# Kernel optimization log

Hardware: AMD Instinct MI355X
Metric: run time of the kernel (lower is better)

## Reference

```python
import jax, jax.numpy as jnp
import numpy as np

# Dimensions (match init_kwargs / input_specs)
B, T, HW, K, J = 8192, 64, 8, 64, 3
FILT_LEN = 8
NEG_SLOPE = 0.001
DWT_OUT_LEN = 84  # lo(14) + hi1(35) + hi2(21) + hi3(14)

# db4 analysis filters (pywt dec_lo / dec_hi)
DB4_LO = np.array([-0.010597401784997278, 0.032883011666982945,
                   0.030841381835986965, -0.18703481171888114,
                   -0.02798376941698385, 0.6308807679295904,
                   0.7148465705525415, 0.23037781330885523], dtype=np.float32)
DB4_HI = np.array([-0.23037781330885523, 0.7148465705525415,
                   -0.6308807679295904, -0.02798376941698385,
                   0.18703481171888114, 0.030841381835986965,
                   0.032883011666982945, -0.010597401784997278], dtype=np.float32)
# pytorch_wavelets stores filters reversed and uses conv1d (cross-correlation)
_H = jnp.asarray(np.ascontiguousarray(np.stack([DB4_LO[::-1], DB4_HI[::-1]])[:, None, :]))  # [2,1,8]


def _afb1d(x):
    # Single-level analysis filter bank along last axis, reflect padding, stride 2.
    # x: [N, n] -> (lo, hi) each [N, floor((n+7)/2)]
    n = x.shape[-1]
    out = (n + FILT_LEN - 1) // 2
    p = 2 * (out - 1) - n + FILT_LEN
    xp = jnp.pad(x, ((0, 0), (p // 2, (p + 1) // 2)), mode='reflect')
    y = jax.lax.conv_general_dilated(xp[:, None, :], _H, (2,), 'VALID')  # [N,2,out]
    return y[:, 0], y[:, 1]


def _dwt(x):
    # J-level DWT; concat [lo_J, hi_1, hi_2, ..., hi_J] along last axis -> [N, 84]
    lo, his = x, []
    for _ in range(J):
        lo, hi = _afb1d(lo)
        his.append(hi)
    return jnp.concatenate([lo] + his, axis=-1)


def setup_inputs() -> dict:
    key = jax.random.key(0)
    k1, k2 = jax.random.split(key)
    x = jax.random.normal(k1, (B, 1, T, HW, HW), dtype=jnp.float32)
    fan_in = DWT_OUT_LEN * HW * HW
    conv_w = jax.random.normal(k2, (K, DWT_OUT_LEN, HW, HW), dtype=jnp.float32) / np.sqrt(fan_in).astype(np.float32)
    conv_b = jnp.zeros((K,), dtype=jnp.float32)
    return {"x": x, "conv_w": conv_w, "conv_b": conv_b}


def reference(x, conv_w, conv_b):
    # x: [B,1,T,H,W]; time_interval=1 and spatial_maxpool_size=1 -> no-ops.
    b = x.shape[0]
    # DWT along time for every (batch, spatial) signal, fully batched.
    sig = x[:, 0].transpose(0, 2, 3, 1).reshape(b * HW * HW, T)  # [B*H*W, T]
    coeffs = _dwt(sig).reshape(b, HW, HW, DWT_OUT_LEN)           # [B,H,W,84]
    # Conv3d with kernel covering the full (84,8,8) volume == one GEMM per output channel.
    feat = jnp.einsum('bhwt,kthw->bk', coeffs, conv_w) + conv_b  # [B,K]
    # Dropout3d in eval mode is identity; LeakyReLU then flatten -> [B, K]
    return jnp.where(feat >= 0, feat, NEG_SLOPE * feat)
```

## Files before the change

kernel.cpp:

```cpp
#include <hip/hip_runtime.h>
#include <hip/hip_bf16.h>

typedef __attribute__((ext_vector_type(4))) float floatx4;
typedef __attribute__((ext_vector_type(8))) short shortx8;

__device__ __constant__ float DLO[8] = {
    -0.010597401784997278f, 0.032883011666982945f,
     0.030841381835986965f, -0.18703481171888114f,
    -0.02798376941698385f,  0.6308807679295904f,
     0.7148465705525415f,   0.23037781330885523f};
__device__ __constant__ float DHI[8] = {
    -0.23037781330885523f,  0.7148465705525415f,
    -0.6308807679295904f,  -0.02798376941698385f,
     0.18703481171888114f,  0.030841381835986965f,
     0.032883011666982945f, -0.010597401784997278f};

__device__ __forceinline__ unsigned short f2bf_rne(float f) {
  unsigned u = __builtin_bit_cast(unsigned, f);
  unsigned r = (u + 0x7FFFu + ((u >> 16) & 1u)) >> 16;
  return (unsigned short)r;
}

template <int N, int OUT>
__device__ __forceinline__ void afb(const float* x, float* lo, float* hi) {
#pragma unroll
  for (int m = 0; m < OUT; ++m) {
    float aL = 0.f, aH = 0.f;
#pragma unroll
    for (int i = 0; i < 8; ++i) {
      int s = 2 * m + 1 - i;
      s = (s < 0) ? -s : s;
      s = (s >= N) ? (2 * N - 2 - s) : s;
      float v = x[s];
      aL = fmaf(DLO[i], v, aL);
      aH = fmaf(DHI[i], v, aH);
    }
    lo[m] = aL; hi[m] = aH;
  }
}

__global__ void build_M_kernel(float* __restrict__ M) {
  const int i = threadIdx.x;
  float sig[64];
#pragma unroll
  for (int t = 0; t < 64; ++t) sig[t] = (t == i) ? 1.f : 0.f;
  float lo1[35], hi1[35], lo2[21], hi2[21], lo3[14], hi3[14];
  afb<64, 35>(sig, lo1, hi1);
  afb<35, 21>(lo1, lo2, hi2);
  afb<21, 14>(lo2, lo3, hi3);
#pragma unroll
  for (int t = 0; t < 14; ++t) M[t * 64 + i] = lo3[t];
#pragma unroll
  for (int t = 0; t < 35; ++t) M[(14 + t) * 64 + i] = hi1[t];
#pragma unroll
  for (int t = 0; t < 21; ++t) M[(49 + t) * 64 + i] = hi2[t];
#pragma unroll
  for (int t = 0; t < 14; ++t) M[(70 + t) * 64 + i] = hi3[t];
}

__global__ __launch_bounds__(256) void build_w2_kernel(
    const float* __restrict__ M, const float* __restrict__ cw,
    unsigned short* __restrict__ W2) {
  __shared__ float Ml[84 * 64];
  __shared__ float Cl[84 * 64];
  const int k = blockIdx.x;
  const float* cwk = cw + (size_t)k * (84 * 64);
  for (int idx = threadIdx.x; idx < 84 * 64; idx += 256) {
    Ml[idx] = M[idx];
    Cl[idx] = cwk[idx];
  }
  __syncthreads();
  const int tp  = blockIdx.y * 16 + (threadIdx.x >> 4);
  const int hw0 = (threadIdx.x & 15) * 4;
  float a0 = 0.f, a1 = 0.f, a2 = 0.f, a3 = 0.f;
#pragma unroll 4
  for (int t = 0; t < 84; ++t) {
    const float mv = Ml[t * 64 + tp];
    const float4 cv = *(const float4*)&Cl[t * 64 + hw0];
    a0 = fmaf(mv, cv.x, a0);
    a1 = fmaf(mv, cv.y, a1);
    a2 = fmaf(mv, cv.z, a2);
    a3 = fmaf(mv, cv.w, a3);
  }
  uint2 pk;
  pk.x = (unsigned)f2bf_rne(a0) | ((unsigned)f2bf_rne(a1) << 16);
  pk.y = (unsigned)f2bf_rne(a2) | ((unsigned)f2bf_rne(a3) << 16);
  *(uint2*)(W2 + (size_t)k * 4096 + tp * 64 + hw0) = pk;
}

#define BM 32
#define BN 64
#define BK 128
#define LDK 136
#define NITER 32

__global__ __launch_bounds__(512) void gemm_kernel(
    const float* __restrict__ A, const unsigned short* __restrict__ W2,
    const float* __restrict__ bias, float* __restrict__ out) {
  __shared__ alignas(16) short As[2][BM * LDK];
  __shared__ alignas(16) short Bs[2][BN * LDK];

  const int tid = threadIdx.x;
  const int b0 = blockIdx.x * BM;

  const int ar = tid >> 4;
  const int ac = (tid & 15) * 8;
  const int bn = tid >> 3;
  const int bc = (tid & 7) * 16;

  const float* aptr = A + (size_t)(b0 + ar) * 4096 + ac;
  const unsigned short* bptr = W2 + (size_t)bn * 4096 + bc;

  const int lane = tid & 63;
  const int wave = tid >> 6;
  const int mt = wave >> 2;
  const int nt = wave & 3;
  const int frow = lane & 15;
  const int fk = (lane >> 4) * 8;

  floatx4 acc = {0.f, 0.f, 0.f, 0.f};

  float4 a0_0 = *(const float4*)(aptr + 0);
  float4 a1_0 = *(const float4*)(aptr + 4);
  uint4  b0_0 = *(const uint4*)(bptr + 0);
  uint4  b1_0 = *(const uint4*)(bptr + 8);
  float4 a0_1 = *(const float4*)(aptr + BK);
  float4 a1_1 = *(const float4*)(aptr + BK + 4);
  uint4  b0_1 = *(const uint4*)(bptr + BK);
  uint4  b1_1 = *(const uint4*)(bptr + BK + 8);

#define GSTEP(S, I)                                                          \
  do {                                                                       \
    shortx8 av;                                                              \
    av[0] = (short)f2bf_rne(a0_##S.x); av[1] = (short)f2bf_rne(a0_##S.y);    \
    av[2] = (short)f2bf_rne(a0_##S.z); av[3] = (short)f2bf_rne(a0_##S.w);    \
    av[4] = (short)f2bf_rne(a1_##S.x); av[5] = (short)f2bf_rne(a1_##S.y);    \
    av[6] = (short)f2bf_rne(a1_##S.z); av[7] = (short)f2bf_rne(a1_##S.w);    \
    *(shortx8*)&As[S][ar * LDK + ac] = av;                                   \
    *(uint4*)&Bs[S][bn * LDK + bc] = b0_##S;                                 \
    *(uint4*)&Bs[S][bn * LDK + bc + 8] = b1_##S;                             \
    __asm__ __volatile__("s_waitcnt lgkmcnt(0)\n\ts_barrier" ::: "memory");  \
    if ((I) + 2 < NITER) {                                                   \
      const int c2 = ((I) + 2) * BK;                                         \
      a0_##S = *(const float4*)(aptr + c2);                                  \
      a1_##S = *(const float4*)(aptr + c2 + 4);                              \
      b0_##S = *(const uint4*)(bptr + c2);                                   \
      b1_##S = *(const uint4*)(bptr + c2 + 8);                               \
    }                                                                        \
    _Pragma("unroll")                                                        \
    for (int kk = 0; kk < 4; ++kk) {                                         \
      shortx8 af = *(const shortx8*)&As[S][(mt * 16 + frow) * LDK + kk * 32 + fk]; \
      shortx8 bf = *(const shortx8*)&Bs[S][(nt * 16 + frow) * LDK + kk * 32 + fk]; \
      acc = __builtin_amdgcn_mfma_f32_16x16x32_bf16(af, bf, acc, 0, 0, 0);   \
    }                                                                        \
  } while (0)

  for (int i = 0; i < NITER; i += 2) {
    GSTEP(0, i);
    GSTEP(1, i + 1);
  }
#undef GSTEP

  const int ocol = nt * 16 + (lane & 15);
  const int orow0 = b0 + mt * 16 + (lane >> 4) * 4;
  const float bv = bias[ocol];
#pragma unroll
  for (int r = 0; r < 4; ++r) {
    float v = acc[r] + bv;
    out[(size_t)(orow0 + r) * 64 + ocol] = (v >= 0.f) ? v : 1.0e-3f * v;
  }
}

extern "C" void kernel_launch(void* const* d_in, const int* in_sizes, int n_in,
                              void* d_out, int out_size, void* d_ws, size_t ws_size,
                              hipStream_t stream) {
  const float* x      = (const float*)d_in[0];
  const float* conv_w = (const float*)d_in[1];
  const float* conv_b = (const float*)d_in[2];
  float* out = (float*)d_out;

  float* Mws = (float*)d_ws;
  unsigned short* W2 = (unsigned short*)((char*)d_ws + 32768);

  build_M_kernel<<<1, 64, 0, stream>>>(Mws);
  build_w2_kernel<<<dim3(64, 4), 256, 0, stream>>>(Mws, conv_w, W2);
  gemm_kernel<<<256, 512, 0, stream>>>(x, W2, conv_b, out);
}
```

Before: 202.8 us.

## Precompute DWT matrix at compile time and use split-K register-direct MFMA GEMM

The DWT basis matrix is now built as a constexpr table in constant memory, so the build_M kernel launch and its global round trip go away. The GEMM is restructured so each 256-thread block handles 16 rows, and its four waves each take a quarter of K. Operands are loaded straight from global memory into MFMA registers, with no LDS staging and no per-step barriers. Partial sums are reduced once through LDS at the end. The change trades LDS tiling for more redundant global reads of W2 (from cache) and a lower in-flight prefetch depth.

New measurement: 220.3 us. +8.7%, slower.

```diff
diff --git a/kernel.cpp b/kernel.cpp
--- a/kernel.cpp
+++ b/kernel.cpp
@@ -4,16 +4,53 @@
 typedef __attribute__((ext_vector_type(4))) float floatx4;
 typedef __attribute__((ext_vector_type(8))) short shortx8;
 
-__device__ __constant__ float DLO[8] = {
+constexpr float CLO[8] = {
     -0.010597401784997278f, 0.032883011666982945f,
      0.030841381835986965f, -0.18703481171888114f,
     -0.02798376941698385f,  0.6308807679295904f,
      0.7148465705525415f,   0.23037781330885523f};
-__device__ __constant__ float DHI[8] = {
+constexpr float CHI[8] = {
     -0.23037781330885523f,  0.7148465705525415f,
     -0.6308807679295904f,  -0.02798376941698385f,
      0.18703481171888114f,  0.030841381835986965f,
      0.032883011666982945f, -0.010597401784997278f};
+
+template <int N, int OUT>
+constexpr void afb_c(const float* x, float* lo, float* hi) {
+  for (int m = 0; m < OUT; ++m) {
+    float aL = 0.f, aH = 0.f;
+    for (int i = 0; i < 8; ++i) {
+      int s = 2 * m + 1 - i;
+      s = (s < 0) ? -s : s;
+      s = (s >= N) ? (2 * N - 2 - s) : s;
+      aL += CLO[i] * x[s];
+      aH += CHI[i] * x[s];
+    }
+    lo[m] = aL; hi[m] = aH;
+  }
+}
+
+struct MTab { float v[84][64]; };
+
+constexpr MTab make_M() {
+  MTab t{};
+  for (int c = 0; c < 64; ++c) {
+    float sig[64] = {};
+    sig[c] = 1.f;
+    float lo1[35] = {}, hi1[35] = {}, lo2[21] = {}, hi2[21] = {};
+    float lo3[14] = {}, hi3[14] = {};
+    afb_c<64, 35>(sig, lo1, hi1);
+    afb_c<35, 21>(lo1, lo2, hi2);
+    afb_c<21, 14>(lo2, lo3, hi3);
+    for (int m = 0; m < 14; ++m) t.v[m][c]      = lo3[m];
+    for (int m = 0; m < 35; ++m) t.v[14 + m][c] = hi1[m];
+    for (int m = 0; m < 21; ++m) t.v[49 + m][c] = hi2[m];
+    for (int m = 0; m < 14; ++m) t.v[70 + m][c] = hi3[m];
+  }
+  return t;
+}
+
+__device__ __constant__ MTab M_TAB = make_M();
 
 __device__ __forceinline__ unsigned short f2bf_rne(float f) {
   unsigned u = __builtin_bit_cast(unsigned, f);
@@ -21,61 +58,19 @@
   return (unsigned short)r;
 }
 
-template <int N, int OUT>
-__device__ __forceinline__ void afb(const float* x, float* lo, float* hi) {
-#pragma unroll
-  for (int m = 0; m < OUT; ++m) {
-    float aL = 0.f, aH = 0.f;
-#pragma unroll
-    for (int i = 0; i < 8; ++i) {
-      int s = 2 * m + 1 - i;
-      s = (s < 0) ? -s : s;
-      s = (s >= N) ? (2 * N - 2 - s) : s;
-      float v = x[s];
-      aL = fmaf(DLO[i], v, aL);
-      aH = fmaf(DHI[i], v, aH);
-    }
-    lo[m] = aL; hi[m] = aH;
-  }
-}
-
-__global__ void build_M_kernel(float* __restrict__ M) {
-  const int i = threadIdx.x;
-  float sig[64];
-#pragma unroll
-  for (int t = 0; t < 64; ++t) sig[t] = (t == i) ? 1.f : 0.f;
-  float lo1[35], hi1[35], lo2[21], hi2[21], lo3[14], hi3[14];
-  afb<64, 35>(sig, lo1, hi1);
-  afb<35, 21>(lo1, lo2, hi2);
-  afb<21, 14>(lo2, lo3, hi3);
-#pragma unroll
-  for (int t = 0; t < 14; ++t) M[t * 64 + i] = lo3[t];
-#pragma unroll
-  for (int t = 0; t < 35; ++t) M[(14 + t) * 64 + i] = hi1[t];
-#pragma unroll
-  for (int t = 0; t < 21; ++t) M[(49 + t) * 64 + i] = hi2[t];
-#pragma unroll
-  for (int t = 0; t < 14; ++t) M[(70 + t) * 64 + i] = hi3[t];
-}
-
 __global__ __launch_bounds__(256) void build_w2_kernel(
-    const float* __restrict__ M, const float* __restrict__ cw,
-    unsigned short* __restrict__ W2) {
-  __shared__ float Ml[84 * 64];
+    const float* __restrict__ cw, unsigned short* __restrict__ W2) {
   __shared__ float Cl[84 * 64];
   const int k = blockIdx.x;
   const float* cwk = cw + (size_t)k * (84 * 64);
-  for (int idx = threadIdx.x; idx < 84 * 64; idx += 256) {
-    Ml[idx] = M[idx];
-    Cl[idx] = cwk[idx];
-  }
+  for (int idx = threadIdx.x; idx < 84 * 64; idx += 256) Cl[idx] = cwk[idx];
   __syncthreads();
   const int tp  = blockIdx.y * 16 + (threadIdx.x >> 4);
   const int hw0 = (threadIdx.x & 15) * 4;
   float a0 = 0.f, a1 = 0.f, a2 = 0.f, a3 = 0.f;
 #pragma unroll 4
   for (int t = 0; t < 84; ++t) {
-    const float mv = Ml[t * 64 + tp];
+    const float mv = M_TAB.v[t][tp];
     const float4 cv = *(const float4*)&Cl[t * 64 + hw0];
     a0 = fmaf(mv, cv.x, a0);
     a1 = fmaf(mv, cv.y, a1);
@@ -88,87 +83,78 @@
   *(uint2*)(W2 + (size_t)k * 4096 + tp * 64 + hw0) = pk;
 }
 
-#define BM 32
-#define BN 64
-#define BK 128
-#define LDK 136
-#define NITER 32
+#define KQ_LEN 1024
+#define KCHUNK 32
 
-__global__ __launch_bounds__(512) void gemm_kernel(
+__global__ __launch_bounds__(256, 2) void gemm_kernel(
     const float* __restrict__ A, const unsigned short* __restrict__ W2,
     const float* __restrict__ bias, float* __restrict__ out) {
-  __shared__ alignas(16) short As[2][BM * LDK];
-  __shared__ alignas(16) short Bs[2][BN * LDK];
+  __shared__ float part[4 * 64 * 16];
 
-  const int tid = threadIdx.x;
-  const int b0 = blockIdx.x * BM;
+  const int tid  = threadIdx.x;
+  const int lane = tid & 63;
+  const int kq   = tid >> 6;
+  const int frow = lane & 15;
+  const int kg   = lane >> 4;
 
-  const int ar = tid >> 4;
-  const int ac = (tid & 15) * 8;
-  const int bn = tid >> 3;
-  const int bc = (tid & 7) * 16;
+  const float* aptr =
+      A + (size_t)(blockIdx.x * 16 + frow) * 4096 + kq * KQ_LEN + kg * 8;
+  const unsigned short* bptr =
+      W2 + (size_t)frow * 4096 + kq * KQ_LEN + kg * 8;
 
-  const float* aptr = A + (size_t)(b0 + ar) * 4096 + ac;
-  const unsigned short* bptr = W2 + (size_t)bn * 4096 + bc;
+  floatx4 acc0 = {0.f, 0.f, 0.f, 0.f};
+  floatx4 acc1 = {0.f, 0.f, 0.f, 0.f};
+  floatx4 acc2 = {0.f, 0.f, 0.f, 0.f};
+  floatx4 acc3 = {0.f, 0.f, 0.f, 0.f};
 
-  const int lane = tid & 63;
-  const int wave = tid >> 6;
-  const int mt = wave >> 2;
-  const int nt = wave & 3;
-  const int frow = lane & 15;
-  const int fk = (lane >> 4) * 8;
+#pragma unroll 2
+  for (int i = 0; i < KQ_LEN / KCHUNK; ++i) {
+    const int off = i * KCHUNK;
+    float4 a0 = *(const float4*)(aptr + off);
+    float4 a1 = *(const float4*)(aptr + off + 4);
+    uint4 bv0 = *(const uint4*)(bptr + off);
+    uint4 bv1 = *(const uint4*)(bptr + 16 * 4096 + off);
+    uint4 bv2 = *(const uint4*)(bptr + 32 * 4096 + off);
+    uint4 bv3 = *(const uint4*)(bptr + 48 * 4096 + off);
+    shortx8 af;
+    af[0] = (short)f2bf_rne(a0.x); af[1] = (short)f2bf_rne(a0.y);
+    af[2] = (short)f2bf_rne(a0.z); af[3] = (short)f2bf_rne(a0.w);
+    af[4] = (short)f2bf_rne(a1.x); af[5] = (short)f2bf_rne(a1.y);
+    af[6] = (short)f2bf_rne(a1.z); af[7] = (short)f2bf_rne(a1.w);
+    acc0 = __builtin_amdgcn_mfma_f32_16x16x32_bf16(
+        af, __builtin_bit_cast(shortx8, bv0), acc0, 0, 0, 0);
+    acc1 = __builtin_amdgcn_mfma_f32_16x16x32_bf16(
+        af, __builtin_bit_cast(shortx8, bv1), acc1, 0, 0, 0);
+    acc2 = __builtin_amdgcn_mfma_f32_16x16x32_bf16(
+        af, __builtin_bit_cast(shortx8, bv2), acc2, 0, 0, 0);
+    acc3 = __builtin_amdgcn_mfma_f32_16x16x32_bf16(
+        af, __builtin_bit_cast(shortx8, bv3), acc3, 0, 0, 0);
+  }
 
-  floatx4 acc = {0.f, 0.f, 0.f, 0.f};
+  float* pp = &part[(kq * 64 + lane) * 16];
+  *(floatx4*)(pp + 0)  = acc0;
+  *(floatx4*)(pp + 4)  = acc1;
+  *(floatx4*)(pp + 8)  = acc2;
+  *(floatx4*)(pp + 12) = acc3;
+  __syncthreads();
 
-  float4 a0_0 = *(const float4*)(aptr + 0);
-  float4 a1_0 = *(const float4*)(aptr + 4);
-  uint4  b0_0 = *(const uint4*)(bptr + 0);
-  uint4  b1_0 = *(const uint4*)(bptr + 8);
-  float4 a0_1 = *(const float4*)(aptr + BK);
-  float4 a1_1 = *(const float4*)(aptr + BK + 4);
-  uint4  b0_1 = *(const uint4*)(bptr + BK);
-  uint4  b1_1 = *(const uint4*)(bptr + BK + 8);
-
-#define GSTEP(S, I)                                                          \
-  do {                                                                       \
-    shortx8 av;                                                              \
-    av[0] = (short)f2bf_rne(a0_##S.x); av[1] = (short)f2bf_rne(a0_##S.y);    \
-    av[2] = (short)f2bf_rne(a0_##S.z); av[3] = (short)f2bf_rne(a0_##S.w);    \
-    av[4] = (short)f2bf_rne(a1_##S.x); av[5] = (short)f2bf_rne(a1_##S.y);    \
-    av[6] = (short)f2bf_rne(a1_##S.z); av[7] = (short)f2bf_rne(a1_##S.w);    \
-    *(shortx8*)&As[S][ar * LDK + ac] = av;                                   \
-    *(uint4*)&Bs[S][bn * LDK + bc] = b0_##S;                                 \
-    *(uint4*)&Bs[S][bn * LDK + bc + 8] = b1_##S;                             \
-    __asm__ __volatile__("s_waitcnt lgkmcnt(0)\n\ts_barrier" ::: "memory");  \
-    if ((I) + 2 < NITER) {                                                   \
-      const int c2 = ((I) + 2) * BK;                                         \
-      a0_##S = *(const float4*)(aptr + c2);                                  \
-      a1_##S = *(const float4*)(aptr + c2 + 4);                              \
-      b0_##S = *(const uint4*)(bptr + c2);                                   \
-      b1_##S = *(const uint4*)(bptr + c2 + 8);                               \
-    }                                                                        \
-    _Pragma("unroll")                                                        \
-    for (int kk = 0; kk < 4; ++kk) {                                         \
-      shortx8 af = *(const shortx8*)&As[S][(mt * 16 + frow) * LDK + kk * 32 + fk]; \
-      shortx8 bf = *(const shortx8*)&Bs[S][(nt * 16 + frow) * LDK + kk * 32 + fk]; \
-      acc = __builtin_amdgcn_mfma_f32_16x16x32_bf16(af, bf, acc, 0, 0, 0);   \
-    }                                                                        \
-  } while (0)
-
-  for (int i = 0; i < NITER; i += 2) {
-    GSTEP(0, i);
-    GSTEP(1, i + 1);
+  const int erow = tid >> 4;
+  const int ecg  = (tid & 15) * 4;
+  const int nt   = ecg >> 4;
+  const int rr   = erow & 3;
+  float4 res;
+  float* rp = (float*)&res;
+#pragma unroll
+  for (int j = 0; j < 4; ++j) {
+    const int c = ecg + j;
+    const int l = ((erow >> 2) << 4) | (c & 15);
+    float s = 0.f;
+#pragma unroll
+    for (int q = 0; q < 4; ++q) s += part[(q * 64 + l) * 16 + nt * 4 + rr];
+    const float v = s + bias[c];
+    rp[j] = (v >= 0.f) ? v : 0.001f * v;
   }
-#undef GSTEP
-
-  const int ocol = nt * 16 + (lane & 15);
-  const int orow0 = b0 + mt * 16 + (lane >> 4) * 4;
-  const float bv = bias[ocol];
-#pragma unroll
-  for (int r = 0; r < 4; ++r) {
-    float v = acc[r] + bv;
-    out[(size_t)(orow0 + r) * 64 + ocol] = (v >= 0.f) ? v : 1.0e-3f * v;
-  }
+  *(float4*)(out + (size_t)(blockIdx.x * 16 + erow) * 64 + ecg) = res;
 }
 
 extern "C" void kernel_launch(void* const* d_in, const int* in_sizes, int n_in,
@@ -179,10 +165,8 @@
   const float* conv_b = (const float*)d_in[2];
   float* out = (float*)d_out;
 
-  float* Mws = (float*)d_ws;
-  unsigned short* W2 = (unsigned short*)((char*)d_ws + 32768);
+  unsigned short* W2 = (unsigned short*)d_ws;
 
-  build_M_kernel<<<1, 64, 0, stream>>>(Mws);
-  build_w2_kernel<<<dim3(64, 4), 256, 0, stream>>>(Mws, conv_w, W2);
-  gemm_kernel<<<256, 512, 0, stream>>>(x, W2, conv_b, out);
+  build_w2_kernel<<<dim3(64, 4), 256, 0, stream>>>(conv_w, W2);
+  gemm_kernel<<<512, 256, 0, stream>>>(x, W2, conv_b, out);
 }
```
